# Performance work log

Measured on AMD Instinct MI355X. Metric: run time of the kernel, lower is better.

The kernel has to match this reference:

```python
import jax, jax.numpy as jnp
import numpy as np

B = 64       # number of graphs (regular batching)
NPER = 2048  # nodes per graph
K = 16       # kNN neighbors (includes self, as torch_cluster.knn does)
D_IN = 64
D_OUT = 64


def setup_inputs() -> dict:
    key = jax.random.key(0)
    k1, k2 = jax.random.split(key, 2)
    x = jax.random.normal(k1, (B * NPER, D_IN), jnp.float32)
    batch = jnp.repeat(jnp.arange(B, dtype=jnp.int32), NPER)
    # MLP: Linear(2*in_channels, out_channels, bias=True) + ReLU
    weight = jax.random.normal(k2, (D_OUT, 2 * D_IN), jnp.float32) * (1.0 / np.sqrt(2 * D_IN))
    bias = jnp.zeros((D_OUT,), jnp.float32)
    return {"x": x, "batch": batch, "weight": weight, "bias": bias}


def reference(x, batch, weight, bias):
    # batch is a regular assignment (NPER nodes per graph) -> block the kNN per graph
    d = x.shape[1]
    xb = x.reshape(B, NPER, d)                                   # [B, n, d]
    # squared euclidean distances within each graph
    sq = jnp.sum(xb * xb, axis=-1)                               # [B, n]
    dist = sq[:, :, None] + sq[:, None, :] - 2.0 * jnp.einsum('bnd,bmd->bnm', xb, xb)
    # k nearest (smallest distance); self-distance 0 -> self included, matching PyG knn
    _, idx = jax.lax.top_k(-dist, K)                             # [B, n, K]
    xj = jax.vmap(lambda feats, ids: feats[ids])(xb, idx)        # [B, n, K, d]
    xi = xb[:, :, None, :]                                        # [B, n, 1, d]
    msg = jnp.concatenate([jnp.broadcast_to(xi, xj.shape), xj - xi], axis=-1)  # [B,n,K,2d]
    h = jax.nn.relu(jnp.einsum('bnkf,of->bnko', msg, weight) + bias)
    out = jnp.max(h, axis=2)                                      # max aggregation over neighbors
    return out.reshape(B * NPER, -1)
```

## Files before the change

### kernel.cpp

```cpp
#include <hip/hip_runtime.h>
#include <cfloat>

#define BB 64
#define NPERB 2048
#define KNN 16
#define NTOT (BB*NPERB)
#define NCAND 24

typedef __bf16 bf16x8 __attribute__((ext_vector_type(8)));
typedef float  f32x4  __attribute__((ext_vector_type(4)));

__device__ __forceinline__ unsigned int med3u(unsigned int a, unsigned int b, unsigned int c) {
    unsigned int d;
    asm("v_med3_u32 %0, %1, %2, %3" : "=v"(d) : "v"(a), "v"(b), "v"(c));
    return d;
}

__device__ __forceinline__ unsigned short bf16rn(float f) {
    unsigned int u = __float_as_uint(f);
    u += 0x7fffu + ((u >> 16) & 1u);
    return (unsigned short)(u >> 16);
}
__device__ __forceinline__ unsigned int pk2(float a, float b) {
    return ((unsigned int)bf16rn(b) << 16) | (unsigned int)bf16rn(a);
}

__global__ __launch_bounds__(256) void k_transform(const float4* __restrict__ x4,
    const float* __restrict__ w, const float* __restrict__ bias,
    float* __restrict__ Aout, float* __restrict__ Bvv, float* __restrict__ sqnp,
    uint4* __restrict__ xbu4)
{
    __shared__ __align__(16) float wm[64*64];
    __shared__ __align__(16) float w2m[64*64];
    const int t = threadIdx.x;
    const int r = blockIdx.x * 256 + t;

#pragma unroll
    for (int i = 0; i < 16; ++i) {
        int e = t + i*256;
        int o = e >> 6, f = e & 63;
        float w1 = w[o*128 + f];
        float w2 = w[o*128 + 64 + f];
        wm[e]  = w1 - w2;
        w2m[e] = w2;
    }

    float xr[64];
#pragma unroll
    for (int j = 0; j < 16; ++j) {
        float4 v = x4[(size_t)r * 16 + j];
        xr[4*j+0] = v.x; xr[4*j+1] = v.y; xr[4*j+2] = v.z; xr[4*j+3] = v.w;
    }

    {
        float rr[8];
#pragma unroll
        for (int j = 0; j < 8; ++j) rr[j] = __fmul_rn(xr[j], xr[j]);
#pragma unroll
        for (int i = 1; i < 8; ++i)
#pragma unroll
            for (int j = 0; j < 8; ++j)
                rr[j] = __fadd_rn(rr[j], __fmul_rn(xr[8*i + j], xr[8*i + j]));
        float t01 = __fadd_rn(rr[0], rr[1]);
        float t23 = __fadd_rn(rr[2], rr[3]);
        float t45 = __fadd_rn(rr[4], rr[5]);
        float t67 = __fadd_rn(rr[6], rr[7]);
        sqnp[r] = __fadd_rn(__fadd_rn(t01, t23), __fadd_rn(t45, t67));
    }

#pragma unroll
    for (int i = 0; i < 8; ++i) {
        uint4 u;
        u.x = pk2(xr[8*i+0], xr[8*i+1]);
        u.y = pk2(xr[8*i+2], xr[8*i+3]);
        u.z = pk2(xr[8*i+4], xr[8*i+5]);
        u.w = pk2(xr[8*i+6], xr[8*i+7]);
        xbu4[(size_t)r * 8 + i] = u;
    }

    __syncthreads();

    for (int o = 0; o < 64; o += 4) {
        float a4[4], b4[4];
#pragma unroll
        for (int oo = 0; oo < 4; ++oo) {
            const float* wmr  = &wm [(o + oo)*64];
            const float* w2mr = &w2m[(o + oo)*64];
            float a1 = 0.f, a2 = 0.f;
#pragma unroll
            for (int fi = 0; fi < 16; ++fi) {
                f32x4 wa = *(const f32x4*)&wmr [fi*4];
                f32x4 wb = *(const f32x4*)&w2mr[fi*4];
#pragma unroll
                for (int k = 0; k < 4; ++k) {
                    float xv = xr[fi*4 + k];
                    a1 = __builtin_fmaf(xv, wa[k], a1);
                    a2 = __builtin_fmaf(xv, wb[k], a2);
                }
            }
            a4[oo] = __fadd_rn(a1, bias[o + oo]);
            b4[oo] = a2;
        }
        *(float4*)&Aout[(size_t)r * 64 + o] = make_float4(a4[0], a4[1], a4[2], a4[3]);
        *(float4*)&Bvv [(size_t)r * 64 + o] = make_float4(b4[0], b4[1], b4[2], b4[3]);
    }
}

__global__ __launch_bounds__(256, 5) void k_topk(const float4* __restrict__ x4,
    const uint4* __restrict__ xb, const float* __restrict__ sq, int* __restrict__ nbr)
{
    __shared__ __align__(16) char smem[28160];
    unsigned short* bsh0 = (unsigned short*)smem;
    unsigned short* bsh1 = (unsigned short*)(smem + 9216);
    unsigned short* rsh  = (unsigned short*)(smem + 18432);
    float* sqc           = (float*)(smem + 27648);
    unsigned int* cand   = (unsigned int*)smem;
    unsigned short* cand24 = (unsigned short*)(smem + 17408);

    int t = threadIdx.x;
    int lane = t & 63;
    int w = t >> 6;
    int ln = lane & 15, qd = lane >> 4;
    int batch = blockIdx.x >> 5;
    int strip = blockIdx.x & 31;
    int rbase = batch * NPERB;
    int r0g = rbase + strip * 64;

    unsigned int ks[16];
#pragma unroll
    for (int j = 0; j < 16; ++j) ks[j] = 0xFFFFFFFFu;

    uint4 p0, p1; float sp;
    auto issue_load = [&](int ct_) {
        const uint4* src = xb + ((size_t)rbase + ct_*64) * 8;
        p0 = src[t]; p1 = src[t + 256];
        sp = (t < 64) ? sq[rbase + ct_*64 + t] : 0.f;
    };
    auto stage_write = [&](int buf_) {
        unsigned short* bnext = buf_ ? bsh1 : bsh0;
        *(uint4*)&bnext[(t >> 3)*72 + (t & 7)*8] = p0;
        int l1 = t + 256;
        *(uint4*)&bnext[(l1 >> 3)*72 + (l1 & 7)*8] = p1;
        if (t < 64) sqc[buf_*64 + t] = sp;
    };

    {
        const uint4* src = xb + (size_t)r0g * 8;
#pragma unroll
        for (int i = 0; i < 2; ++i) {
            int l = t + i*256;
            uint4 v = src[l];
            *(uint4*)&rsh[(l >> 3)*72 + (l & 7)*8] = v;
        }
    }
    issue_load(0);
    __syncthreads();
    bf16x8 rf0 = *(const bf16x8*)&rsh[(w*16 + ln)*72 + qd*8];
    bf16x8 rf1 = *(const bf16x8*)&rsh[(w*16 + ln)*72 + 32 + qd*8];
    float sqr16 = sq[r0g + w*16 + ln] + 16.f;
    stage_write(0);
    issue_load(1);
    __syncthreads();

    for (int ct = 0; ct < 32; ++ct) {
        if (ct < 31) stage_write((ct + 1) & 1);
        if (ct < 30) issue_load(ct + 2);
        const unsigned short* bcur = (ct & 1) ? bsh1 : bsh0;
        const float* sqcur = sqc + (ct & 1)*64;
#pragma unroll
        for (int ct2 = 0; ct2 < 4; ++ct2) {
            int pt = ct2*16 + ln;
            bf16x8 a0 = *(const bf16x8*)&bcur[pt*72 + qd*8];
            bf16x8 a1 = *(const bf16x8*)&bcur[pt*72 + 32 + qd*8];
            f32x4 acc = {0.f, 0.f, 0.f, 0.f};
            acc = __builtin_amdgcn_mfma_f32_16x16x32_bf16(a0, rf0, acc, 0, 0, 0);
            acc = __builtin_amdgcn_mfma_f32_16x16x32_bf16(a1, rf1, acc, 0, 0, 0);
            f32x4 sc4 = *(const f32x4*)&sqcur[ct2*16 + qd*4];
            int idxb = ct*64 + ct2*16 + qd*4;
#pragma unroll
            for (int j = 0; j < 4; ++j) {
                float s = fmaf(-2.f, acc[j], sc4[j] + sqr16);
                unsigned int u = (__float_as_uint(s) & 0xFFFFF800u) | (unsigned int)(idxb + j);
#pragma unroll
                for (int jj = 15; jj >= 1; --jj) ks[jj] = med3u(u, ks[jj-1], ks[jj]);
                ks[0] = min(ks[0], u);
            }
        }
        __syncthreads();
    }

    {
        int r = w*16 + ln;
#pragma unroll
        for (int j = 0; j < 16; ++j) cand[r*68 + qd*16 + j] = ks[j];
    }
    __syncthreads();

    if (t < 64) {
        unsigned int m24[NCAND];
#pragma unroll
        for (int j = 0; j < NCAND; ++j) m24[j] = 0xFFFFFFFFu;
        for (int i = 0; i < 64; ++i) {
            unsigned int u = cand[t*68 + i];
#pragma unroll
            for (int jj = NCAND-1; jj >= 1; --jj) m24[jj] = med3u(u, m24[jj-1], m24[jj]);
            m24[0] = min(m24[0], u);
        }
#pragma unroll
        for (int j = 0; j < NCAND; ++j) cand24[t*NCAND + j] = (unsigned short)(m24[j] & 0x7FFu);
    }
    __syncthreads();

    {
        int r = t & 63, grp = t >> 6;
        float sqr = sq[r0g + r];
        float4 xrA[8];
#pragma unroll
        for (int i = 0; i < 8; ++i) xrA[i] = x4[(size_t)(r0g + r)*16 + i];
        float* kdf = (float*)cand;
#pragma unroll
        for (int m6 = 0; m6 < 6; ++m6) {
            int m = grp*6 + m6;
            int c = (int)cand24[r*NCAND + m];
            const float4* xb4 = &x4[(size_t)(rbase + c)*16];
            float dot = 0.f;
#pragma unroll
            for (int i = 0; i < 8; ++i) {
                float4 a = xrA[i]; float4 b = xb4[i];
                dot = fmaf(a.x, b.x, dot); dot = fmaf(a.y, b.y, dot);
                dot = fmaf(a.z, b.z, dot); dot = fmaf(a.w, b.w, dot);
            }
#pragma unroll
            for (int i = 8; i < 16; ++i) {
                float4 a = x4[(size_t)(r0g + r)*16 + i]; float4 b = xb4[i];
                dot = fmaf(a.x, b.x, dot); dot = fmaf(a.y, b.y, dot);
                dot = fmaf(a.z, b.z, dot); dot = fmaf(a.w, b.w, dot);
            }
            float kd = __fsub_rn(__fadd_rn(sqr, sq[rbase + c]), __fmul_rn(2.0f, dot));
            kdf[r*68 + m] = kd;
            cand[r*68 + 32 + m] = (unsigned int)c;
        }
    }
    __syncthreads();

    if (t < 64) {
        float* kdf = (float*)cand;
        float dk[KNN]; int di[KNN];
#pragma unroll
        for (int j = 0; j < KNN; ++j) { dk[j] = FLT_MAX; di[j] = 0x7fffffff; }
        for (int m = 0; m < NCAND; ++m) {
            float kd = kdf[t*68 + m];
            int c = (int)cand[t*68 + 32 + m];
            bool better = (kd < dk[KNN-1]) || (kd == dk[KNN-1] && c < di[KNN-1]);
            if (better) {
#pragma unroll
                for (int j = KNN-1; j >= 1; --j) {
                    bool sh = (dk[j-1] > kd) || (dk[j-1] == kd && di[j-1] > c);
                    bool pl = (!sh) && ((dk[j] > kd) || (dk[j] == kd && di[j] > c));
                    float nk = sh ? dk[j-1] : (pl ? kd : dk[j]);
                    int ni = sh ? di[j-1] : (pl ? c : di[j]);
                    dk[j] = nk; di[j] = ni;
                }
                if ((dk[0] > kd) || (dk[0] == kd && di[0] > c)) { dk[0] = kd; di[0] = c; }
            }
        }
#pragma unroll
        for (int k = 0; k < KNN; ++k) nbr[(size_t)(r0g + t)*16 + k] = di[k];
    }
}

__global__ __launch_bounds__(256) void k_combine(const float* __restrict__ Bvv,
    const int* __restrict__ nbr, float* __restrict__ out)
{
    int t = threadIdx.x;
    int row = blockIdx.x*4 + (t >> 6);
    int o = t & 63;
    int rb = (row >> 11) << 11;
    float m = -FLT_MAX;
#pragma unroll
    for (int k = 0; k < 16; ++k) {
        int c = nbr[(size_t)row*16 + k];
        m = fmaxf(m, Bvv[(size_t)(rb + c)*64 + o]);
    }
    out[(size_t)row*64 + o] = fmaxf(out[(size_t)row*64 + o] + m, 0.f);
}

extern "C" void kernel_launch(void* const* d_in, const int* in_sizes, int n_in,
                              void* d_out, int out_size, void* d_ws, size_t ws_size,
                              hipStream_t stream) {
    const float* x    = (const float*)d_in[0];
    const float* w    = (const float*)d_in[2];
    const float* bias = (const float*)d_in[3];
    float* out = (float*)d_out;

    float* Bvv  = (float*)d_ws;
    float* sqnp = Bvv + (size_t)NTOT * 64;
    int*   nbr  = (int*)(sqnp + NTOT);
    unsigned int* xbu = (unsigned int*)(nbr + (size_t)NTOT * 16);

    k_transform<<<NTOT/256, 256, 0, stream>>>((const float4*)x, w, bias, out, Bvv, sqnp, (uint4*)xbu);
    k_topk<<<2048, 256, 0, stream>>>((const float4*)x, (const uint4*)xbu, sqnp, nbr);
    k_combine<<<NTOT/4, 256, 0, stream>>>(Bvv, nbr, out);
}
```

Baseline: 530.2 us.

## Load top-k tiles directly into LDS with XOR swizzle instead of register staging

Replaces the register-staged double buffering of candidate tiles and squared norms with direct global-to-LDS loads, issued one tile ahead into the alternate buffer. The padded 72-element row layout becomes a dense 64-element layout with an XOR swizzle on 16-byte chunks, which avoids bank conflicts and shrinks shared memory. The aim is to cut staging registers and VALU/LDS store instructions in the hot loop. In exchange, the prefetch distance drops from two tiles to one, and correctness depends on the barrier waiting for the async LDS loads.

```diff
diff --git a/kernel.cpp b/kernel.cpp
--- a/kernel.cpp
+++ b/kernel.cpp
@@ -109,11 +109,11 @@
 __global__ __launch_bounds__(256, 5) void k_topk(const float4* __restrict__ x4,
     const uint4* __restrict__ xb, const float* __restrict__ sq, int* __restrict__ nbr)
 {
-    __shared__ __align__(16) char smem[28160];
+    __shared__ __align__(16) char smem[26112];
     unsigned short* bsh0 = (unsigned short*)smem;
-    unsigned short* bsh1 = (unsigned short*)(smem + 9216);
-    unsigned short* rsh  = (unsigned short*)(smem + 18432);
-    float* sqc           = (float*)(smem + 27648);
+    unsigned short* bsh1 = (unsigned short*)(smem + 8192);
+    unsigned short* rsh  = (unsigned short*)(smem + 16384);
+    float* sqc           = (float*)(smem + 25600);
     unsigned int* cand   = (unsigned int*)smem;
     unsigned short* cand24 = (unsigned short*)(smem + 17408);
 
@@ -130,18 +130,25 @@
 #pragma unroll
     for (int j = 0; j < 16; ++j) ks[j] = 0xFFFFFFFFu;
 
-    uint4 p0, p1; float sp;
-    auto issue_load = [&](int ct_) {
-        const uint4* src = xb + ((size_t)rbase + ct_*64) * 8;
-        p0 = src[t]; p1 = src[t + 256];
-        sp = (t < 64) ? sq[rbase + ct_*64 + t] : 0.f;
-    };
-    auto stage_write = [&](int buf_) {
-        unsigned short* bnext = buf_ ? bsh1 : bsh0;
-        *(uint4*)&bnext[(t >> 3)*72 + (t & 7)*8] = p0;
-        int l1 = t + 256;
-        *(uint4*)&bnext[(l1 >> 3)*72 + (l1 & 7)*8] = p1;
-        if (t < 64) sqc[buf_*64 + t] = sp;
+    const int rowl = lane >> 3;
+    const int c16s = (lane & 7) ^ (rowl & 7);
+    auto issue_tile = [&](int ct_, int buf_) {
+        char* base = smem + buf_*8192;
+#pragma unroll
+        for (int i = 0; i < 2; ++i) {
+            int seg = w*2 + i;
+            int row = seg*8 + rowl;
+            const uint4* src = xb + ((size_t)rbase + ct_*64 + row)*8 + c16s;
+            __builtin_amdgcn_global_load_lds(
+                (const __attribute__((address_space(1))) void*)src,
+                (__attribute__((address_space(3))) void*)(base + seg*1024), 16, 0, 0);
+        }
+        if (w == 0) {
+            const float* ssrc = sq + rbase + ct_*64 + lane;
+            __builtin_amdgcn_global_load_lds(
+                (const __attribute__((address_space(1))) void*)ssrc,
+                (__attribute__((address_space(3))) void*)(sqc + buf_*64), 4, 0, 0);
+        }
     };
 
     {
@@ -153,25 +160,22 @@
             *(uint4*)&rsh[(l >> 3)*72 + (l & 7)*8] = v;
         }
     }
-    issue_load(0);
+    issue_tile(0, 0);
     __syncthreads();
     bf16x8 rf0 = *(const bf16x8*)&rsh[(w*16 + ln)*72 + qd*8];
     bf16x8 rf1 = *(const bf16x8*)&rsh[(w*16 + ln)*72 + 32 + qd*8];
     float sqr16 = sq[r0g + w*16 + ln] + 16.f;
-    stage_write(0);
-    issue_load(1);
-    __syncthreads();
 
     for (int ct = 0; ct < 32; ++ct) {
-        if (ct < 31) stage_write((ct + 1) & 1);
-        if (ct < 30) issue_load(ct + 2);
+        if (ct < 31) issue_tile(ct + 1, (ct + 1) & 1);
         const unsigned short* bcur = (ct & 1) ? bsh1 : bsh0;
         const float* sqcur = sqc + (ct & 1)*64;
 #pragma unroll
         for (int ct2 = 0; ct2 < 4; ++ct2) {
             int pt = ct2*16 + ln;
-            bf16x8 a0 = *(const bf16x8*)&bcur[pt*72 + qd*8];
-            bf16x8 a1 = *(const bf16x8*)&bcur[pt*72 + 32 + qd*8];
+            int sw = pt & 7;
+            bf16x8 a0 = *(const bf16x8*)&bcur[pt*64 + ((qd       ^ sw) * 8)];
+            bf16x8 a1 = *(const bf16x8*)&bcur[pt*64 + (((qd + 4) ^ sw) * 8)];
             f32x4 acc = {0.f, 0.f, 0.f, 0.f};
             acc = __builtin_amdgcn_mfma_f32_16x16x32_bf16(a0, rf0, acc, 0, 0, 0);
             acc = __builtin_amdgcn_mfma_f32_16x16x32_bf16(a1, rf1, acc, 0, 0, 0);
```

Measured after the change: 558.4 us. +5.3%, slower.
